# Performance work log

Measured on AMD Instinct MI355X. Metric: run time of the kernel, lower is better.

The kernel has to match this reference:

```python
import jax, jax.numpy as jnp
import numpy as np

B, C, E, H = 4, 2048, 1024, 16
D = E // H
EPS = 1e-5

def _layernorm(x, g, b):
    mu = jnp.mean(x, axis=-1, keepdims=True)
    var = jnp.mean(jnp.square(x - mu), axis=-1, keepdims=True)
    return (x - mu) * jax.lax.rsqrt(var + EPS) * g + b

def setup_inputs() -> dict:
    key = jax.random.key(0)
    ks = jax.random.split(key, 12)
    s = 1.0 / np.sqrt(E)
    return {
        "inputs": jax.random.normal(ks[0], (B, C, E), dtype=jnp.float32),
        "Wq": jax.random.normal(ks[1], (E, E), dtype=jnp.float32) * s,
        "bq": jnp.zeros((E,), dtype=jnp.float32),
        "Wk": jax.random.normal(ks[2], (E, E), dtype=jnp.float32) * s,
        "bk": jnp.zeros((E,), dtype=jnp.float32),
        "Wv": jax.random.normal(ks[3], (E, E), dtype=jnp.float32) * s,
        "bv": jnp.zeros((E,), dtype=jnp.float32),
        "g1": jnp.ones((E,), dtype=jnp.float32),
        "beta1": jnp.zeros((E,), dtype=jnp.float32),
        "g2": jnp.ones((E,), dtype=jnp.float32),
        "beta2": jnp.zeros((E,), dtype=jnp.float32),
        "W1": jax.random.normal(ks[4], (E, 4 * E), dtype=jnp.float32) * s,
        "bm1": jnp.zeros((4 * E,), dtype=jnp.float32),
        "W2": jax.random.normal(ks[5], (4 * E, E), dtype=jnp.float32) * (1.0 / np.sqrt(4 * E)),
        "bm2": jnp.zeros((E,), dtype=jnp.float32),
    }

def reference(inputs, Wq, bq, Wk, bk, Wv, bv, g1, beta1, g2, beta2, W1, bm1, W2, bm2):
    b, c, e = inputs.shape
    normed = _layernorm(inputs, g1, beta1)
    q = (normed @ Wq + bq).reshape(b, c, H, D).transpose(0, 2, 1, 3)  # [B,H,C,D]
    k = (normed @ Wk + bk).reshape(b, c, H, D).transpose(0, 2, 1, 3)
    v = (normed @ Wv + bv).reshape(b, c, H, D).transpose(0, 2, 1, 3)
    scores = jnp.einsum('bhqd,bhkd->bhqk', q, k) / np.sqrt(D).astype(np.float32)
    causal = jnp.triu(jnp.ones((c, c), dtype=bool), k=1)  # True above diagonal
    scores = jnp.where(causal, -jnp.inf, scores)
    probs = jax.nn.softmax(scores, axis=-1)
    attn = jnp.einsum('bhqk,bhkd->bhqd', probs, v)
    attn = attn.transpose(0, 2, 1, 3).reshape(b, c, e)
    out = inputs + attn
    h = _layernorm(out, g2, beta2)
    mlp = jax.nn.relu(h @ W1 + bm1) @ W2 + bm2
    return out + mlp
```

## Files before the change

### kernel.cpp

```cpp
#include <hip/hip_runtime.h>
#include <math.h>

#define B_ 4
#define C_ 2048
#define E_ 1024
#define H_ 16
#define D_ 64
#define ROWS_ (B_*C_)

typedef __bf16 bf16x8 __attribute__((ext_vector_type(8)));
typedef float f32x4 __attribute__((ext_vector_type(4)));

__device__ __forceinline__ float b2f(unsigned short u) {
  unsigned int x = ((unsigned int)u) << 16;
  return __builtin_bit_cast(float, x);
}
__device__ __forceinline__ unsigned short f2b(float f) {
  unsigned int x = __builtin_bit_cast(unsigned int, f);
  unsigned int r = (x + 0x7FFFu + ((x >> 16) & 1u)) >> 16;
  return (unsigned short)r;
}
__device__ __forceinline__ unsigned short tob(float f) { return f2b(f); }
__device__ __forceinline__ unsigned short tob(unsigned short u) { return u; }
__device__ __forceinline__ void store_out(float* p, float v) { *p = v; }
__device__ __forceinline__ void store_out(unsigned short* p, float v) { *p = f2b(v); }

__device__ __forceinline__ void async16(const void* g, void* l) {
  __builtin_amdgcn_global_load_lds(
      (__attribute__((address_space(1))) unsigned int*)g,
      (__attribute__((address_space(3))) unsigned int*)l, 16, 0, 0);
}

template <typename InT>
__global__ __launch_bounds__(256) void transpose64(
    const InT* __restrict__ in, unsigned short* __restrict__ out,
    int s_in, int s_out, int Hz, long zs_b, long zs_h, long zs_out)
{
  __shared__ unsigned short t[64][65];
  int z = blockIdx.z;
  long ib = (long)(z / Hz) * zs_b + (long)(z % Hz) * zs_h;
  long ob = (long)z * zs_out;
  int r0 = blockIdx.y * 64, c0 = blockIdx.x * 64;
  int lane = threadIdx.x & 63, grp = threadIdx.x >> 6;
  for (int i = grp; i < 64; i += 4)
    t[i][lane] = tob(in[ib + (long)(r0 + i) * s_in + c0 + lane]);
  __syncthreads();
  for (int i = grp; i < 64; i += 4)
    out[ob + (long)(c0 + i) * s_out + r0 + lane] = t[lane][i];
}

__global__ void concat_bias(const float* __restrict__ q,
                            const float* __restrict__ k,
                            const float* __restrict__ v,
                            float* __restrict__ o)
{
  int i = blockIdx.x * 256 + threadIdx.x;
  o[i] = (i < 1024) ? q[i] : (i < 2048) ? k[i - 1024] : v[i - 2048];
}

__global__ __launch_bounds__(256) void ln_kernel(
    const float* __restrict__ xin, const unsigned short* __restrict__ addend,
    const float* __restrict__ g, const float* __restrict__ beta,
    unsigned short* __restrict__ yout, float* __restrict__ out1)
{
  int row = blockIdx.x, tid = threadIdx.x;
  size_t base = (size_t)row * E_ + tid * 4;
  float4 xa = *(const float4*)(xin + base);
  float v0 = xa.x, v1 = xa.y, v2 = xa.z, v3 = xa.w;
  if (addend) {
    ushort4 aa = *(const ushort4*)(addend + base);
    v0 += b2f(aa.x); v1 += b2f(aa.y); v2 += b2f(aa.z); v3 += b2f(aa.w);
  }
  if (out1) {
    *(float4*)(out1 + base) = make_float4(v0, v1, v2, v3);
  }
  float s = v0 + v1 + v2 + v3;
  float sq = v0*v0 + v1*v1 + v2*v2 + v3*v3;
  #pragma unroll
  for (int off = 32; off >= 1; off >>= 1) {
    s  += __shfl_xor(s, off);
    sq += __shfl_xor(sq, off);
  }
  __shared__ float red[8];
  int wid = tid >> 6;
  if ((tid & 63) == 0) { red[wid] = s; red[4 + wid] = sq; }
  __syncthreads();
  s  = red[0] + red[1] + red[2] + red[3];
  sq = red[4] + red[5] + red[6] + red[7];
  float mu = s * (1.0f / E_);
  float var = sq * (1.0f / E_) - mu * mu;
  float rs = rsqrtf(var + 1e-5f);
  float4 ga = *(const float4*)(g + tid * 4);
  float4 ba = *(const float4*)(beta + tid * 4);
  ushort4 o;
  o.x = f2b((v0 - mu) * rs * ga.x + ba.x);
  o.y = f2b((v1 - mu) * rs * ga.y + ba.y);
  o.z = f2b((v2 - mu) * rs * ga.z + ba.z);
  o.w = f2b((v3 - mu) * rs * ga.w + ba.w);
  *(ushort4*)(yout + base) = o;
}

#define BARC() { asm volatile("" ::: "memory"); __builtin_amdgcn_s_barrier(); asm volatile("" ::: "memory"); }

#define MFMA_Q(mh) do {                                                     \
  __builtin_amdgcn_s_setprio(1);                                            \
  _Pragma("unroll")                                                         \
  for (int mt_ = 0; mt_ < 4; ++mt_)                                         \
    _Pragma("unroll")                                                       \
    for (int nt_ = 0; nt_ < 4; ++nt_)                                       \
      acc[(mh)*4+mt_][nt_] = __builtin_amdgcn_mfma_f32_16x16x32_bf16(       \
          af[mt_], bfr[nt_], acc[(mh)*4+mt_][nt_], 0, 0, 0);                \
  __builtin_amdgcn_s_setprio(0);                                            \
} while (0)

template <typename OutT>
__global__ __launch_bounds__(512, 2) void gemm256(
    const unsigned short* __restrict__ A, const unsigned short* __restrict__ Bt,
    const float* __restrict__ bias, const float* __restrict__ resid,
    OutT* __restrict__ Co, int M, int N, int K, int lda, int ldb,
    int relu, size_t zs)
{
  __shared__ __align__(16) unsigned short As[2][256 * 64];
  __shared__ __align__(16) unsigned short Bs[2][256 * 64];
  int tid = threadIdx.x, lane = tid & 63, wid = tid >> 6;
  int lane15 = lane & 15, quad = lane >> 4;
  int wm = wid >> 2, wn = wid & 3;

  int i = blockIdx.x;
  int xcd = i & 7, c = i >> 3;
  int bm = xcd * 4 + (c & 3);
  int bn = c >> 2;
  size_t koff = (size_t)blockIdx.z * K;
  int z0 = (blockIdx.z == 0);
  Co += (size_t)blockIdx.z * zs;

  int sr = tid >> 3, sc = tid & 7;
  int gcol = (sc ^ (sr & 7)) * 8;
  const unsigned short* Ag = A + koff + (size_t)(bm * 256 + sr) * lda + gcol;
  const unsigned short* Bg = Bt + koff + (size_t)(bn * 256 + sr) * ldb + gcol;
  int dstb = wid * 512;

  int NT = K >> 6;

  f32x4 acc[8][4];
  #pragma unroll
  for (int m = 0; m < 8; ++m)
    #pragma unroll
    for (int n = 0; n < 4; ++n) acc[m][n] = 0.0f;

  auto stage = [&](int kt) {
    unsigned short* Ad = &As[kt & 1][dstb];
    unsigned short* Bd = &Bs[kt & 1][dstb];
    const unsigned short* Asrc = Ag + kt * 64;
    const unsigned short* Bsrc = Bg + kt * 64;
    #pragma unroll
    for (int h = 0; h < 4; ++h) {
      async16(Asrc + (size_t)(h * 64) * lda, Ad + h * 4096);
      async16(Bsrc + (size_t)(h * 64) * ldb, Bd + h * 4096);
    }
  };
  int rsw = lane15 & 7;

  stage(0);
  asm volatile("s_waitcnt vmcnt(0)" ::: "memory");
  __builtin_amdgcn_s_barrier();

  for (int t = 0; t < NT; ++t) {
    const unsigned short* Ab = &As[t & 1][0];
    const unsigned short* Bb = &Bs[t & 1][0];
    if (t + 1 < NT) stage(t + 1);
    __builtin_amdgcn_sched_barrier(0);
    bf16x8 af[4], bfr[4];
    #pragma unroll
    for (int m = 0; m < 4; ++m)
      af[m] = *(const bf16x8*)&Ab[(wm * 128 + m * 16 + lane15) * 64 + ((quad ^ rsw) * 8)];
    #pragma unroll
    for (int n = 0; n < 4; ++n)
      bfr[n] = *(const bf16x8*)&Bb[(wn * 64 + n * 16 + lane15) * 64 + ((quad ^ rsw) * 8)];
    MFMA_Q(0);
    __builtin_amdgcn_sched_barrier(0);
    #pragma unroll
    for (int m = 0; m < 4; ++m)
      af[m] = *(const bf16x8*)&Ab[(wm * 128 + 64 + m * 16 + lane15) * 64 + ((quad ^ rsw) * 8)];
    MFMA_Q(1);
    __builtin_amdgcn_sched_barrier(0);
    #pragma unroll
    for (int m = 0; m < 4; ++m)
      af[m] = *(const bf16x8*)&Ab[(wm * 128 + m * 16 + lane15) * 64 + (((4 + quad) ^ rsw) * 8)];
    #pragma unroll
    for (int n = 0; n < 4; ++n)
      bfr[n] = *(const bf16x8*)&Bb[(wn * 64 + n * 16 + lane15) * 64 + (((4 + quad) ^ rsw) * 8)];
    MFMA_Q(0);
    __builtin_amdgcn_sched_barrier(0);
    #pragma unroll
    for (int m = 0; m < 4; ++m)
      af[m] = *(const bf16x8*)&Ab[(wm * 128 + 64 + m * 16 + lane15) * 64 + (((4 + quad) ^ rsw) * 8)];
    MFMA_Q(1);
    asm volatile("s_waitcnt vmcnt(0)" ::: "memory");
    BARC();
  }

  #pragma unroll
  for (int nt = 0; nt < 4; ++nt) {
    int col = bn * 256 + wn * 64 + nt * 16 + lane15;
    float bv = (bias && z0) ? bias[col] : 0.0f;
    #pragma unroll
    for (int mt = 0; mt < 8; ++mt) {
      int row0 = bm * 256 + wm * 128 + mt * 16 + quad * 4;
      #pragma unroll
      for (int r = 0; r < 4; ++r) {
        float val = acc[mt][nt][r] + bv;
        if (relu) val = fmaxf(val, 0.0f);
        if (resid && z0) val += resid[(size_t)(row0 + r) * N + col];
        store_out(&Co[(size_t)(row0 + r) * N + col], val);
      }
    }
  }
}

__global__ __launch_bounds__(256) void add2(
    const float* __restrict__ p0, const float* __restrict__ p1,
    float* __restrict__ out)
{
  size_t i = ((size_t)blockIdx.x * 256 + threadIdx.x) * 4;
  float4 a = *(const float4*)(p0 + i);
  float4 b = *(const float4*)(p1 + i);
  *(float4*)(out + i) = make_float4(a.x + b.x, a.y + b.y, a.z + b.z, a.w + b.w);
}

__global__ __launch_bounds__(512) void attn_kernel(
    const unsigned short* __restrict__ qkv, const unsigned short* __restrict__ vt,
    unsigned short* __restrict__ attnb,
    float* __restrict__ opart0, float* __restrict__ opart1,
    float* __restrict__ lpart)
{
  __shared__ __align__(16) unsigned short Klds[64 * 64];
  __shared__ __align__(16) unsigned short Vlds[64 * 64];
  __shared__ __align__(16) unsigned short Plds[8][16 * 72];
  int tid = threadIdx.x, lane = tid & 63, widx = tid >> 6;
  int lane15 = lane & 15, quad = lane >> 4;

  int bx = blockIdx.x;
  int qblk, p, split;
  if (bx < 16) { qblk = 15 - (bx >> 1); p = bx & 1; split = 1; }
  else         { qblk = 23 - bx;        p = 0;      split = 0; }
  int ntiles = 2 * qblk + 2;
  int kt0 = (split && p) ? (qblk + 1) : 0;
  int kt1 = (split && !p) ? (qblk + 1) : ntiles;

  int bh = blockIdx.y;
  int b = bh >> 4, h = bh & 15;
  int q0w = qblk * 128 + widx * 16;

  const float QSCALE = 0.18033688011112042f;
  const unsigned short* qb = qkv + (size_t)(b * C_ + q0w + lane15) * 3072 + h * 64;
  bf16x8 qa0 = *(const bf16x8*)(qb + quad * 8);
  bf16x8 qa1 = *(const bf16x8*)(qb + 32 + quad * 8);
  #pragma unroll
  for (int j = 0; j < 8; ++j) {
    qa0[j] = (__bf16)((float)qa0[j] * QSCALE);
    qa1[j] = (__bf16)((float)qa1[j] * QSCALE);
  }

  float lsum[4];
  f32x4 o[4];
  #pragma unroll
  for (int r = 0; r < 4; ++r) lsum[r] = 0.0f;
  #pragma unroll
  for (int nt = 0; nt < 4; ++nt) o[nt] = 0.0f;

  int sr = tid >> 3, sc = tid & 7, sw = sr & 7;
  const unsigned short* kg = qkv + (size_t)(b * C_ + kt0 * 64 + sr) * 3072 + 1024 + h * 64 + (sc ^ sw) * 8;
  const unsigned short* vg = vt + (size_t)bh * 64 * 2048 + (size_t)sr * 2048 + (sc ^ sw) * 8 + kt0 * 64;
  unsigned short* kl = &Klds[sr * 64 + sc * 8];
  unsigned short* vl = &Vlds[sr * 64 + sc * 8];
  int swr = lane15 & 7;

  for (int kt = kt0; kt < kt1; ++kt) {
    int k0 = kt * 64;
    async16(kg, kl);
    async16(vg, vl);
    kg += (size_t)64 * 3072;
    vg += 64;
    __syncthreads();

    if (k0 <= q0w + 15) {
      f32x4 s[4];
      #pragma unroll
      for (int g = 0; g < 4; ++g) s[g] = 0.0f;
      #pragma unroll
      for (int g = 0; g < 4; ++g) {
        int row = g * 16 + lane15;
        bf16x8 kf0 = *(const bf16x8*)&Klds[row * 64 + ((quad ^ swr) * 8)];
        bf16x8 kf1 = *(const bf16x8*)&Klds[row * 64 + (((4 + quad) ^ swr) * 8)];
        s[g] = __builtin_amdgcn_mfma_f32_16x16x32_bf16(qa0, kf0, s[g], 0, 0, 0);
        s[g] = __builtin_amdgcn_mfma_f32_16x16x32_bf16(qa1, kf1, s[g], 0, 0, 0);
      }

      if (k0 + 63 > q0w) {
        #pragma unroll
        for (int g = 0; g < 4; ++g)
          #pragma unroll
          for (int r = 0; r < 4; ++r)
            if (k0 + g * 16 + lane15 > q0w + quad * 4 + r) s[g][r] = -3.0e38f;
      }

      float pv[4][4];
      #pragma unroll
      for (int g = 0; g < 4; ++g)
        #pragma unroll
        for (int r = 0; r < 4; ++r) pv[g][r] = exp2f(s[g][r]);
      #pragma unroll
      for (int r = 0; r < 4; ++r)
        lsum[r] += (pv[0][r] + pv[1][r]) + (pv[2][r] + pv[3][r]);

      __bf16* prow = (__bf16*)&Plds[widx][0];
      #pragma unroll
      for (int g = 0; g < 4; ++g)
        #pragma unroll
        for (int r = 0; r < 4; ++r)
          prow[(quad * 4 + r) * 72 + g * 16 + lane15] = (__bf16)pv[g][r];
      asm volatile("s_waitcnt lgkmcnt(0)" ::: "memory");
      bf16x8 pa0 = *(const bf16x8*)&Plds[widx][lane15 * 72 + quad * 8];
      bf16x8 pa1 = *(const bf16x8*)&Plds[widx][lane15 * 72 + 32 + quad * 8];

      #pragma unroll
      for (int nt = 0; nt < 4; ++nt) {
        int d = nt * 16 + lane15;
        bf16x8 vf0 = *(const bf16x8*)&Vlds[d * 64 + ((quad ^ swr) * 8)];
        bf16x8 vf1 = *(const bf16x8*)&Vlds[d * 64 + (((4 + quad) ^ swr) * 8)];
        o[nt] = __builtin_amdgcn_mfma_f32_16x16x32_bf16(pa0, vf0, o[nt], 0, 0, 0);
        o[nt] = __builtin_amdgcn_mfma_f32_16x16x32_bf16(pa1, vf1, o[nt], 0, 0, 0);
      }
    }
    __syncthreads();
  }

  #pragma unroll
  for (int off = 1; off <= 8; off <<= 1)
    #pragma unroll
    for (int r = 0; r < 4; ++r)
      lsum[r] += __shfl_xor(lsum[r], off);

  if (!split) {
    float rl[4];
    #pragma unroll
    for (int r = 0; r < 4; ++r) rl[r] = 1.0f / lsum[r];
    #pragma unroll
    for (int nt = 0; nt < 4; ++nt)
      #pragma unroll
      for (int r = 0; r < 4; ++r) {
        float val = o[nt][r] * rl[r];
        attnb[(size_t)(b * C_ + q0w + quad * 4 + r) * E_ + h * 64 + nt * 16 + lane15] = f2b(val);
      }
  } else {
    float* op = p ? opart1 : opart0;
    size_t rbase = (size_t)bh * 1024 + (q0w - 1024) + quad * 4;
    #pragma unroll
    for (int nt = 0; nt < 4; ++nt)
      #pragma unroll
      for (int r = 0; r < 4; ++r)
        op[(rbase + r) * 64 + nt * 16 + lane15] = o[nt][r];
    if (lane15 == 0) {
      float* lp = lpart + (size_t)p * 65536;
      #pragma unroll
      for (int r = 0; r < 4; ++r) lp[rbase + r] = lsum[r];
    }
  }
}

__global__ __launch_bounds__(256) void attn_combine(
    const float* __restrict__ opart0, const float* __restrict__ opart1,
    const float* __restrict__ lpart, unsigned short* __restrict__ attnb)
{
  size_t i = (size_t)blockIdx.x * 256 + threadIdx.x;
  int d = (int)(i & 63);
  size_t rowi = i >> 6;
  int bh = (int)(rowi >> 10), row = (int)(rowi & 1023);
  float ov = opart0[rowi * 64 + d] + opart1[rowi * 64 + d];
  float lv = lpart[rowi] + lpart[65536 + rowi];
  int b = bh >> 4, h = bh & 15;
  attnb[(size_t)(b * C_ + 1024 + row) * E_ + h * 64 + d] = f2b(ov / lv);
}

extern "C" void kernel_launch(void* const* d_in, const int* in_sizes, int n_in,
                              void* d_out, int out_size, void* d_ws, size_t ws_size,
                              hipStream_t stream)
{
  const float* x   = (const float*)d_in[0];
  const float* Wq  = (const float*)d_in[1];
  const float* bq  = (const float*)d_in[2];
  const float* Wk  = (const float*)d_in[3];
  const float* bk  = (const float*)d_in[4];
  const float* Wv  = (const float*)d_in[5];
  const float* bv  = (const float*)d_in[6];
  const float* g1  = (const float*)d_in[7];
  const float* be1 = (const float*)d_in[8];
  const float* g2  = (const float*)d_in[9];
  const float* be2 = (const float*)d_in[10];
  const float* W1  = (const float*)d_in[11];
  const float* bm1 = (const float*)d_in[12];
  const float* W2  = (const float*)d_in[13];
  const float* bm2 = (const float*)d_in[14];

  char* ws = (char*)d_ws;
  float*          part0 = (float*)(ws + 0);
  unsigned short* norm1 = (unsigned short*)(ws + 0);
  unsigned short* wT    = (unsigned short*)(ws + 16777216);
  unsigned short* w1T   = (unsigned short*)(ws + 23068672);
  float*          biasq = (float*)(ws + 39845888);
  unsigned short* qkv   = (unsigned short*)(ws + 39858176);
  unsigned short* vtb   = (unsigned short*)(ws + 90189824);
  unsigned short* mid   = (unsigned short*)(ws + 39858176);
  unsigned short* attnb = (unsigned short*)(ws + 106967040);
  float*          out1  = (float*)(ws + 123744256);
  unsigned short* w2T   = (unsigned short*)(ws + 157298688);
  float*          part1 = (float*)(ws + 165687296);
  float*          opart0 = (float*)(ws + 165687296);
  float*          opart1 = (float*)(ws + 123744256);
  float*          lpartb = (float*)(ws + 0);
  size_t part_zs = ((size_t)165687296) / 4;

  transpose64<float><<<dim3(16, 16, 1), 256, 0, stream>>>(Wq, wT,               1024, 1024, 1, 0, 0, 0);
  transpose64<float><<<dim3(16, 16, 1), 256, 0, stream>>>(Wk, wT + 1024 * 1024, 1024, 1024, 1, 0, 0, 0);
  transpose64<float><<<dim3(16, 16, 1), 256, 0, stream>>>(Wv, wT + 2048 * 1024, 1024, 1024, 1, 0, 0, 0);
  transpose64<float><<<dim3(64, 16, 1), 256, 0, stream>>>(W1, w1T, 4096, 1024, 1, 0, 0, 0);
  transpose64<float><<<dim3(16, 64, 1), 256, 0, stream>>>(W2, w2T, 1024, 4096, 1, 0, 0, 0);
  concat_bias<<<12, 256, 0, stream>>>(bq, bk, bv, biasq);

  ln_kernel<<<ROWS_, 256, 0, stream>>>(x, nullptr, g1, be1, norm1, nullptr);

  gemm256<unsigned short><<<dim3(384, 1, 1), 512, 0, stream>>>(
      norm1, wT, biasq, nullptr, qkv, 8192, 3072, 1024, 1024, 1024, 0, 0);

  transpose64<unsigned short><<<dim3(1, 32, 64), 256, 0, stream>>>(
      qkv + 2048, vtb, 3072, 2048, 16, (long)C_ * 3072, 64, (long)64 * 2048);

  attn_kernel<<<dim3(24, 64), 512, 0, stream>>>(qkv, vtb, attnb, opart0, opart1, lpartb);
  attn_combine<<<16384, 256, 0, stream>>>(opart0, opart1, lpartb, attnb);

  ln_kernel<<<ROWS_, 256, 0, stream>>>(x, attnb, g2, be2, norm1, out1);

  gemm256<unsigned short><<<dim3(512, 1, 1), 512, 0, stream>>>(
      norm1, w1T, bm1, nullptr, mid, 8192, 4096, 1024, 1024, 1024, 1, 0);

  gemm256<float><<<dim3(128, 1, 2), 512, 0, stream>>>(
      mid, w2T, bm2, out1, part0, 8192, 1024, 2048, 4096, 4096, 0, part_zs);
  add2<<<8192, 256, 0, stream>>>(part0, part1, (float*)d_out);
}
```

Measured before the change: 565.9 us.

## Double-buffer attention K/V tiles and reorder GEMM fragment loads ahead of MFMAs

The attention kernel now keeps two LDS buffers for K and V. It issues the next tile's async copies before computing the current one, waiting with vmcnt(2) instead of a full sync, so global loads overlap the QK and PV MFMAs. The GEMM inner loop uses separate fragment registers for each A/B quarter, so LDS reads for the next MFMA group are issued before the current group runs. The loop is also kept rolled. This costs more LDS in attention and more VGPRs in the GEMM, which could hurt occupancy under the 512x2 launch bound.

```diff
diff --git a/kernel.cpp b/kernel.cpp
--- a/kernel.cpp
+++ b/kernel.cpp
@@ -101,15 +101,16 @@
 }
 
 #define BARC() { asm volatile("" ::: "memory"); __builtin_amdgcn_s_barrier(); asm volatile("" ::: "memory"); }
-
-#define MFMA_Q(mh) do {                                                     \
+#define SB0() __builtin_amdgcn_sched_barrier(0)
+
+#define MFMA16(mh, AF, BF) do {                                             \
   __builtin_amdgcn_s_setprio(1);                                            \
   _Pragma("unroll")                                                         \
   for (int mt_ = 0; mt_ < 4; ++mt_)                                         \
     _Pragma("unroll")                                                       \
     for (int nt_ = 0; nt_ < 4; ++nt_)                                       \
       acc[(mh)*4+mt_][nt_] = __builtin_amdgcn_mfma_f32_16x16x32_bf16(       \
-          af[mt_], bfr[nt_], acc[(mh)*4+mt_][nt_], 0, 0, 0);                \
+          AF[mt_], BF[nt_], acc[(mh)*4+mt_][nt_], 0, 0, 0);                 \
   __builtin_amdgcn_s_setprio(0);                                            \
 } while (0)
 
@@ -138,7 +139,7 @@
   int gcol = (sc ^ (sr & 7)) * 8;
   const unsigned short* Ag = A + koff + (size_t)(bm * 256 + sr) * lda + gcol;
   const unsigned short* Bg = Bt + koff + (size_t)(bn * 256 + sr) * ldb + gcol;
-  int dstb = wid * 512;
+  int dst = tid * 8;
 
   int NT = K >> 6;
 
@@ -149,8 +150,8 @@
     for (int n = 0; n < 4; ++n) acc[m][n] = 0.0f;
 
   auto stage = [&](int kt) {
-    unsigned short* Ad = &As[kt & 1][dstb];
-    unsigned short* Bd = &Bs[kt & 1][dstb];
+    unsigned short* Ad = &As[kt & 1][0] + dst;
+    unsigned short* Bd = &Bs[kt & 1][0] + dst;
     const unsigned short* Asrc = Ag + kt * 64;
     const unsigned short* Bsrc = Bg + kt * 64;
     #pragma unroll
@@ -160,42 +161,47 @@
     }
   };
   int rsw = lane15 & 7;
+  auto ldA = [&](const unsigned short* Ab, int mh, int m, int kk) {
+    return *(const bf16x8*)&Ab[(wm * 128 + mh * 64 + m * 16 + lane15) * 64
+                               + (((kk * 4 + quad) ^ rsw) * 8)];
+  };
+  auto ldB = [&](const unsigned short* Bb, int n, int kk) {
+    return *(const bf16x8*)&Bb[(wn * 64 + n * 16 + lane15) * 64
+                               + (((kk * 4 + quad) ^ rsw) * 8)];
+  };
 
   stage(0);
   asm volatile("s_waitcnt vmcnt(0)" ::: "memory");
   __builtin_amdgcn_s_barrier();
 
+  #pragma unroll 1
   for (int t = 0; t < NT; ++t) {
     const unsigned short* Ab = &As[t & 1][0];
     const unsigned short* Bb = &Bs[t & 1][0];
     if (t + 1 < NT) stage(t + 1);
-    __builtin_amdgcn_sched_barrier(0);
-    bf16x8 af[4], bfr[4];
-    #pragma unroll
-    for (int m = 0; m < 4; ++m)
-      af[m] = *(const bf16x8*)&Ab[(wm * 128 + m * 16 + lane15) * 64 + ((quad ^ rsw) * 8)];
-    #pragma unroll
-    for (int n = 0; n < 4; ++n)
-      bfr[n] = *(const bf16x8*)&Bb[(wn * 64 + n * 16 + lane15) * 64 + ((quad ^ rsw) * 8)];
-    MFMA_Q(0);
-    __builtin_amdgcn_sched_barrier(0);
-    #pragma unroll
-    for (int m = 0; m < 4; ++m)
-      af[m] = *(const bf16x8*)&Ab[(wm * 128 + 64 + m * 16 + lane15) * 64 + ((quad ^ rsw) * 8)];
-    MFMA_Q(1);
-    __builtin_amdgcn_sched_barrier(0);
-    #pragma unroll
-    for (int m = 0; m < 4; ++m)
-      af[m] = *(const bf16x8*)&Ab[(wm * 128 + m * 16 + lane15) * 64 + (((4 + quad) ^ rsw) * 8)];
-    #pragma unroll
-    for (int n = 0; n < 4; ++n)
-      bfr[n] = *(const bf16x8*)&Bb[(wn * 64 + n * 16 + lane15) * 64 + (((4 + quad) ^ rsw) * 8)];
-    MFMA_Q(0);
-    __builtin_amdgcn_sched_barrier(0);
-    #pragma unroll
-    for (int m = 0; m < 4; ++m)
-      af[m] = *(const bf16x8*)&Ab[(wm * 128 + 64 + m * 16 + lane15) * 64 + (((4 + quad) ^ rsw) * 8)];
-    MFMA_Q(1);
+    bf16x8 b0[4], b1[4], a0[4], a1[4], a2[4], a3[4];
+    #pragma unroll
+    for (int n = 0; n < 4; ++n) b0[n] = ldB(Bb, n, 0);
+    #pragma unroll
+    for (int m = 0; m < 4; ++m) a0[m] = ldA(Ab, 0, m, 0);
+    #pragma unroll
+    for (int m = 0; m < 4; ++m) a1[m] = ldA(Ab, 1, m, 0);
+    SB0();
+    MFMA16(0, a0, b0);
+    SB0();
+    #pragma unroll
+    for (int n = 0; n < 4; ++n) b1[n] = ldB(Bb, n, 1);
+    #pragma unroll
+    for (int m = 0; m < 4; ++m) a2[m] = ldA(Ab, 0, m, 1);
+    SB0();
+    MFMA16(1, a1, b0);
+    SB0();
+    #pragma unroll
+    for (int m = 0; m < 4; ++m) a3[m] = ldA(Ab, 1, m, 1);
+    SB0();
+    MFMA16(0, a2, b1);
+    SB0();
+    MFMA16(1, a3, b1);
     asm volatile("s_waitcnt vmcnt(0)" ::: "memory");
     BARC();
   }
@@ -234,8 +240,8 @@
     float* __restrict__ opart0, float* __restrict__ opart1,
     float* __restrict__ lpart)
 {
-  __shared__ __align__(16) unsigned short Klds[64 * 64];
-  __shared__ __align__(16) unsigned short Vlds[64 * 64];
+  __shared__ __align__(16) unsigned short Klds[2][64 * 64];
+  __shared__ __align__(16) unsigned short Vlds[2][64 * 64];
   __shared__ __align__(16) unsigned short Plds[8][16 * 72];
   int tid = threadIdx.x, lane = tid & 63, widx = tid >> 6;
   int lane15 = lane & 15, quad = lane >> 4;
@@ -272,17 +278,30 @@
   int sr = tid >> 3, sc = tid & 7, sw = sr & 7;
   const unsigned short* kg = qkv + (size_t)(b * C_ + kt0 * 64 + sr) * 3072 + 1024 + h * 64 + (sc ^ sw) * 8;
   const unsigned short* vg = vt + (size_t)bh * 64 * 2048 + (size_t)sr * 2048 + (sc ^ sw) * 8 + kt0 * 64;
-  unsigned short* kl = &Klds[sr * 64 + sc * 8];
-  unsigned short* vl = &Vlds[sr * 64 + sc * 8];
+  unsigned short* kl = &Klds[0][sr * 64 + sc * 8];
+  unsigned short* vl = &Vlds[0][sr * 64 + sc * 8];
   int swr = lane15 & 7;
 
+  async16(kg, kl);
+  async16(vg, vl);
+  kg += (size_t)64 * 3072;
+  vg += 64;
+
   for (int kt = kt0; kt < kt1; ++kt) {
+    int cur = (kt - kt0) & 1;
     int k0 = kt * 64;
-    async16(kg, kl);
-    async16(vg, vl);
-    kg += (size_t)64 * 3072;
-    vg += 64;
-    __syncthreads();
+    bool morek = (kt + 1 < kt1);
+    if (morek) {
+      async16(kg, kl + (cur ^ 1) * 4096);
+      async16(vg, vl + (cur ^ 1) * 4096);
+      kg += (size_t)64 * 3072;
+      vg += 64;
+      asm volatile("s_waitcnt vmcnt(2)" ::: "memory");
+    } else {
+      asm volatile("s_waitcnt vmcnt(0)" ::: "memory");
+    }
+    __builtin_amdgcn_s_barrier();
+    asm volatile("" ::: "memory");
 
     if (k0 <= q0w + 15) {
       f32x4 s[4];
@@ -291,8 +310,8 @@
       #pragma unroll
       for (int g = 0; g < 4; ++g) {
         int row = g * 16 + lane15;
-        bf16x8 kf0 = *(const bf16x8*)&Klds[row * 64 + ((quad ^ swr) * 8)];
-        bf16x8 kf1 = *(const bf16x8*)&Klds[row * 64 + (((4 + quad) ^ swr) * 8)];
+        bf16x8 kf0 = *(const bf16x8*)&Klds[cur][row * 64 + ((quad ^ swr) * 8)];
+        bf16x8 kf1 = *(const bf16x8*)&Klds[cur][row * 64 + (((4 + quad) ^ swr) * 8)];
         s[g] = __builtin_amdgcn_mfma_f32_16x16x32_bf16(qa0, kf0, s[g], 0, 0, 0);
         s[g] = __builtin_amdgcn_mfma_f32_16x16x32_bf16(qa1, kf1, s[g], 0, 0, 0);
       }
@@ -327,13 +346,15 @@
       #pragma unroll
       for (int nt = 0; nt < 4; ++nt) {
         int d = nt * 16 + lane15;
-        bf16x8 vf0 = *(const bf16x8*)&Vlds[d * 64 + ((quad ^ swr) * 8)];
-        bf16x8 vf1 = *(const bf16x8*)&Vlds[d * 64 + (((4 + quad) ^ swr) * 8)];
+        bf16x8 vf0 = *(const bf16x8*)&Vlds[cur][d * 64 + ((quad ^ swr) * 8)];
+        bf16x8 vf1 = *(const bf16x8*)&Vlds[cur][d * 64 + (((4 + quad) ^ swr) * 8)];
         o[nt] = __builtin_amdgcn_mfma_f32_16x16x32_bf16(pa0, vf0, o[nt], 0, 0, 0);
         o[nt] = __builtin_amdgcn_mfma_f32_16x16x32_bf16(pa1, vf1, o[nt], 0, 0, 0);
       }
     }
-    __syncthreads();
+    asm volatile("" ::: "memory");
+    __builtin_amdgcn_s_barrier();
+    asm volatile("" ::: "memory");
   }
 
   #pragma unroll
```

New measurement: 574.5 us. About the same (+1.5%).
